# Performance work log

Hardware: AMD Instinct MI355X
Metric: run time of the kernel (lower is better)

## Reference

```python
import jax, jax.numpy as jnp
import numpy as np

N_NODES = 100000
N_EDGES = 1000000
IN_DIM = 64
OUT_DIM = 64


def setup_inputs() -> dict:
    key = jax.random.key(0)
    k1, k2, k3 = jax.random.split(key, 3)
    x = jax.random.normal(k1, (N_NODES, IN_DIM), dtype=jnp.float32)
    edge_index = jax.random.randint(k2, (2, N_EDGES), 0, N_NODES, dtype=jnp.int64)
    # PyG GCNConv linear weight [out_dim, in_dim] (glorot-ish scale) and bias
    W = jax.random.normal(k3, (OUT_DIM, IN_DIM), dtype=jnp.float32) * (1.0 / np.sqrt(IN_DIM))
    b = jnp.zeros((OUT_DIM,), dtype=jnp.float32)
    return {"x": x, "edge_index": edge_index, "W": W, "b": b}


def reference(x, edge_index, W, b):
    # GCNConv: add self-loops, symmetric deg^{-1/2} normalization,
    # linear transform, scatter-add aggregation, bias.
    # Dropout is identity in eval mode.
    N = x.shape[0]
    loop = jnp.arange(N, dtype=edge_index.dtype)
    src = jnp.concatenate([edge_index[0], loop])  # [E+N]
    dst = jnp.concatenate([edge_index[1], loop])  # [E+N]

    deg = jax.ops.segment_sum(jnp.ones_like(dst, dtype=x.dtype), dst, num_segments=N)
    dinv = jnp.where(deg > 0, jax.lax.rsqrt(deg), 0.0)  # [N]
    norm = dinv[src] * dinv[dst]                         # [E+N]

    h = x @ W.T                                          # [N, out_dim]
    msg = h[src] * norm[:, None]                         # gather + scale
    out = jax.ops.segment_sum(msg, dst, num_segments=N)  # scatter-add
    return out + b
```

## Files before the change

kernel.cpp:

```cpp
#include <hip/hip_runtime.h>

#define DIM 64
#define BIN_SHIFT 7
#define NODES_PER_BIN 128
#define MAX_BINS 1024
#define BIN_CAP 2048
#define CHUNK_EDGES 4096
#define SCATTER_THREADS 1024
#define GEMM_ROWS 128
#define FXSCALE 65536.0f
#define FXINV (1.0f / 65536.0f)
#define FXBIAS 524288u
#define MAGIC 12582912.0f
#define MAGIC_I 0x4B400000u
#define ACC_U64 33


using bf16x8 = __attribute__((ext_vector_type(8))) short;
using u16x8  = __attribute__((ext_vector_type(8))) unsigned short;
using f32x4  = __attribute__((ext_vector_type(4))) float;

__device__ __forceinline__ unsigned short f2bf(float f) {
    unsigned u = __float_as_uint(f);
    u += 0x7fffu + ((u >> 16) & 1u);
    return (unsigned short)(u >> 16);
}
__device__ __forceinline__ float bf2f(unsigned short u) {
    return __uint_as_float((unsigned)u << 16);
}
__device__ __forceinline__ unsigned fxq(unsigned short bf) {
    return __float_as_uint(fmaf(bf2f(bf), FXSCALE, MAGIC)) - (MAGIC_I - FXBIAS);
}

__global__ __launch_bounds__(SCATTER_THREADS) void bin_scatter_kernel(
    const void* __restrict__ ei, int* __restrict__ gcur,
    int* __restrict__ pairs, int E, int nbins) {
    __shared__ int h1[MAX_BINS];
    __shared__ int h2[MAX_BINS];
    __shared__ int base[MAX_BINS];
    __shared__ int s_notz;
    int tid = threadIdx.x;
    if (tid == 0) s_notz = 0;
    for (int i = tid; i < nbins; i += SCATTER_THREADS) { h1[i] = 0; h2[i] = 0; }
    __syncthreads();
    if (((const int*)ei)[2 * tid + 1] != 0) s_notz = 1;
    __syncthreads();
    int is64 = (s_notz == 0);
    int chunk = blockIdx.x * CHUNK_EDGES;

    int ss[CHUNK_EDGES / SCATTER_THREADS], dd[CHUNK_EDGES / SCATTER_THREADS];
#pragma unroll
    for (int k = 0; k < CHUNK_EDGES / SCATTER_THREADS; ++k) {
        int i = chunk + k * SCATTER_THREADS + tid;
        if (i < E) {
            int s, d;
            if (is64) {
                s = (int)((const long long*)ei)[i];
                d = (int)((const long long*)ei)[(long long)i + E];
            } else {
                s = ((const int*)ei)[i];
                d = ((const int*)ei)[i + E];
            }
            ss[k] = s; dd[k] = d;
            atomicAdd(&h1[d >> BIN_SHIFT], 1);
        } else {
            dd[k] = -1;
        }
    }
    __syncthreads();

    int myc = 0, ret = 0;
    if (tid < nbins) {
        myc = h1[tid];
        if (myc) ret = atomicAdd(&gcur[tid], myc);
    }
    int rk[CHUNK_EDGES / SCATTER_THREADS];
#pragma unroll
    for (int k = 0; k < CHUNK_EDGES / SCATTER_THREADS; ++k)
        if (dd[k] >= 0) rk[k] = atomicAdd(&h2[dd[k] >> BIN_SHIFT], 1);
    if (myc) base[tid] = tid * BIN_CAP + ret;
    __syncthreads();

#pragma unroll
    for (int k = 0; k < CHUNK_EDGES / SCATTER_THREADS; ++k) {
        if (dd[k] >= 0) {
            int bin = dd[k] >> BIN_SHIFT;
            int pos = base[bin] + rk[k];
            if (pos < (bin + 1) * BIN_CAP)
                pairs[pos] = (ss[k] << BIN_SHIFT) | (dd[k] & (NODES_PER_BIN - 1));
        }
    }
}

__global__ __launch_bounds__(256) void deg_gemm_kernel(
    const float* __restrict__ x, const float* __restrict__ W,
    const int* __restrict__ pairs, const int* __restrict__ gcur,
    int* __restrict__ deg, float* __restrict__ dinv,
    unsigned short* __restrict__ h, int N) {
    __shared__ unsigned short Xs[GEMM_ROWS * 64];
    __shared__ unsigned short Ws[64 * 64];
    __shared__ int sdeg[NODES_PER_BIN];
    __shared__ float sdinv[NODES_PER_BIN];
    int tid = threadIdx.x;
    int b = blockIdx.x;
    int row0 = b << BIN_SHIFT;
    int nn = min(GEMM_ROWS, N - row0);
    int cntb = min(gcur[b], BIN_CAP);

    if (tid < NODES_PER_BIN) sdeg[tid] = 0;
#pragma unroll
    for (int u = 0; u < 2; ++u) {
        int idx = u * 256 + tid;
        int c = idx >> 3, k0 = (idx & 7) * 8;
        float4 a = *(const float4*)&W[c * 64 + k0];
        float4 bb = *(const float4*)&W[c * 64 + k0 + 4];
        bf16x8 v;
        v[0] = (short)f2bf(a.x); v[1] = (short)f2bf(a.y);
        v[2] = (short)f2bf(a.z); v[3] = (short)f2bf(a.w);
        v[4] = (short)f2bf(bb.x); v[5] = (short)f2bf(bb.y);
        v[6] = (short)f2bf(bb.z); v[7] = (short)f2bf(bb.w);
        int byteoff = c * 128 + ((k0 * 2) ^ ((c & 7) << 4));
        *(bf16x8*)((char*)Ws + byteoff) = v;
    }
    const float* xbase = x + (size_t)row0 * DIM;
#pragma unroll
    for (int u = 0; u < 4; ++u) {
        int idx = u * 256 + tid;
        int r = idx >> 3, k0 = (idx & 7) * 8;
        float4 a = make_float4(0.f, 0.f, 0.f, 0.f), bb = a;
        if (r < nn) {
            a = *(const float4*)&xbase[r * DIM + k0];
            bb = *(const float4*)&xbase[r * DIM + k0 + 4];
        }
        bf16x8 v;
        v[0] = (short)f2bf(a.x); v[1] = (short)f2bf(a.y);
        v[2] = (short)f2bf(a.z); v[3] = (short)f2bf(a.w);
        v[4] = (short)f2bf(bb.x); v[5] = (short)f2bf(bb.y);
        v[6] = (short)f2bf(bb.z); v[7] = (short)f2bf(bb.w);
        int byteoff = r * 128 + ((k0 * 2) ^ ((r & 7) << 4));
        *(bf16x8*)((char*)Xs + byteoff) = v;
    }
    __syncthreads();
    const int* pb = pairs + b * BIN_CAP;
    for (int i = tid; i < cntb; i += 256)
        atomicAdd(&sdeg[pb[i] & (NODES_PER_BIN - 1)], 1);
    __syncthreads();
    if (tid < NODES_PER_BIN) {
        int d = sdeg[tid];
        float dv = rsqrtf((float)(d + 1));
        sdinv[tid] = dv;
        if (tid < nn) {
            deg[row0 + tid] = d;
            dinv[row0 + tid] = dv;
        }
    }
    __syncthreads();

    int w = tid >> 6, l = tid & 63;
    int lm = l & 15, kg = l >> 4;
    f32x4 acc[2][4] = {};
#pragma unroll
    for (int ks = 0; ks < 2; ++ks) {
        int kbyte = ks * 64 + kg * 16;
        int r0g = 32 * w + lm;
        int r1g = 32 * w + 16 + lm;
        bf16x8 a0 = *(const bf16x8*)((const char*)Xs + r0g * 128 + (kbyte ^ ((r0g & 7) << 4)));
        bf16x8 a1 = *(const bf16x8*)((const char*)Xs + r1g * 128 + (kbyte ^ ((r1g & 7) << 4)));
#pragma unroll
        for (int nt = 0; nt < 4; ++nt) {
            int ng = nt * 16 + lm;
            bf16x8 bv = *(const bf16x8*)((const char*)Ws + ng * 128 + (kbyte ^ ((ng & 7) << 4)));
            acc[0][nt] = __builtin_amdgcn_mfma_f32_16x16x32_bf16(a0, bv, acc[0][nt], 0, 0, 0);
            acc[1][nt] = __builtin_amdgcn_mfma_f32_16x16x32_bf16(a1, bv, acc[1][nt], 0, 0, 0);
        }
    }
#pragma unroll
    for (int mt = 0; mt < 2; ++mt) {
#pragma unroll
        for (int j = 0; j < 4; ++j) {
            int rl = 32 * w + 16 * mt + (l >> 4) * 4 + j;
            if (rl < nn) {
                float dv = sdinv[rl];
                size_t rowoff = (size_t)(row0 + rl) * DIM;
#pragma unroll
                for (int nt = 0; nt < 4; ++nt)
                    h[rowoff + nt * 16 + lm] = f2bf(acc[mt][nt][j] * dv);
            }
        }
    }
}

__global__ __launch_bounds__(512) void aggregate_kernel(
    const unsigned short* __restrict__ h, const int* __restrict__ pairs,
    const int* __restrict__ gcur, const int* __restrict__ deg,
    const float* __restrict__ dinv, const float* __restrict__ bias,
    float* __restrict__ out, int N) {
    __shared__ unsigned long long acc[NODES_PER_BIN * ACC_U64];
    int b = blockIdx.x;
    int tid = threadIdx.x;
    int cnt = min(gcur[b], BIN_CAP);
    int node0 = b << BIN_SHIFT;
    int nn = min(NODES_PER_BIN, N - node0);

    for (int i = tid; i < NODES_PER_BIN * ACC_U64; i += 512) acc[i] = 0ULL;
    __syncthreads();

    int wave = tid >> 6, lane = tid & 63;
    int g = lane >> 3;
    int fq = lane & 7;
    const int* pb = pairs + b * BIN_CAP;
    int dummy = N << BIN_SHIFT;

    for (int j0 = 64 * wave; j0 < cnt; j0 += 512) {
        int pk[8]; bool vd[8];
#pragma unroll
        for (int u = 0; u < 8; ++u) {
            int e = j0 + 8 * u + g;
            vd[u] = (e < cnt);
            pk[u] = vd[u] ? pb[e] : dummy;
        }
        u16x8 r[8];
#pragma unroll
        for (int u = 0; u < 8; ++u)
            r[u] = *(const u16x8*)(h + (size_t)(pk[u] >> BIN_SHIFT) * DIM + 8 * fq);
#pragma unroll
        for (int u = 0; u < 8; ++u) {
            unsigned q0 = fxq(r[u][0]), q1 = fxq(r[u][1]);
            unsigned q2 = fxq(r[u][2]), q3 = fxq(r[u][3]);
            unsigned q4 = fxq(r[u][4]), q5 = fxq(r[u][5]);
            unsigned q6 = fxq(r[u][6]), q7 = fxq(r[u][7]);
            if (vd[u]) {
                unsigned long long* ar =
                    &acc[(pk[u] & (NODES_PER_BIN - 1)) * ACC_U64 + 4 * fq];
                atomicAdd(&ar[0], (unsigned long long)q0 | ((unsigned long long)q1 << 32));
                atomicAdd(&ar[1], (unsigned long long)q2 | ((unsigned long long)q3 << 32));
                atomicAdd(&ar[2], (unsigned long long)q4 | ((unsigned long long)q5 << 32));
                atomicAdd(&ar[3], (unsigned long long)q6 | ((unsigned long long)q7 << 32));
            }
        }
    }
    __syncthreads();

    const int* accd = (const int*)acc;
    float bl = bias[lane];
    for (int n0 = wave; n0 < nn; n0 += 8) {
        int gn = node0 + n0;
        int dgn = deg[gn];
        float di = dinv[gn];
        unsigned q = (unsigned)accd[n0 * (2 * ACC_U64) + lane];
        int sfx = (int)(q - (unsigned)dgn * FXBIAS);
        float sum = (float)sfx * FXINV;
        float self = bf2f(h[(size_t)gn * DIM + lane]);
        out[(size_t)gn * DIM + lane] = (sum + self) * di + bl;
    }
}

extern "C" void kernel_launch(void* const* d_in, const int* in_sizes, int n_in,
                              void* d_out, int out_size, void* d_ws, size_t ws_size,
                              hipStream_t stream) {
    const float* x = (const float*)d_in[0];
    const void* ei = d_in[1];
    const float* W = (const float*)d_in[2];
    const float* b = (const float*)d_in[3];
    float* out = (float*)d_out;

    int N = in_sizes[0] / DIM;
    int E = in_sizes[1] / 2;
    int nbins = (N + NODES_PER_BIN - 1) >> BIN_SHIFT;

    char* ws = (char*)d_ws;
    auto align256 = [](size_t v) { return (v + 255) & ~(size_t)255; };
    size_t off = 0;
    int* gcur = (int*)(ws + off);              off = align256(off + (size_t)MAX_BINS * 4);
    int* deg  = (int*)(ws + off);              off = align256(off + (size_t)(N + 1) * 4);
    float* dinv = (float*)(ws + off);          off = align256(off + (size_t)(N + 1) * 4);
    int* pairs = (int*)(ws + off);             off = align256(off + ((size_t)nbins * BIN_CAP + 64) * 4);
    unsigned short* h = (unsigned short*)(ws + off); off = align256(off + (size_t)(N + 1) * DIM * 2);

    int nchunks = (E + CHUNK_EDGES - 1) / CHUNK_EDGES;

    hipMemsetAsync(gcur, 0, (size_t)MAX_BINS * 4, stream);
    bin_scatter_kernel<<<nchunks, SCATTER_THREADS, 0, stream>>>(ei, gcur, pairs, E, nbins);
    deg_gemm_kernel<<<nbins, 256, 0, stream>>>(x, W, pairs, gcur, deg, dinv, h, N);
    aggregate_kernel<<<nbins, 512, 0, stream>>>(h, pairs, gcur, deg, dinv, b, out, N);
}
```

Measured before the change: 126.6 us.

## Fuse scatter, GEMM and aggregation into one cooperative persistent kernel

Replaces the memset plus three-kernel pipeline with a single cooperative kernel that uses grid-wide syncs between the binning, degree/GEMM and aggregation phases. One block per bin also does its share of edge binning and computes the GEMM before the first grid sync, so that work overlaps with the scatter. Degree and dinv stay in shared memory rather than global arrays. The cost is three grid barriers, occupancy limited so every bin fits co-resident, and a fallback to the old path if cooperative launch is unavailable.

```diff
diff --git a/kernel.cpp b/kernel.cpp
--- a/kernel.cpp
+++ b/kernel.cpp
@@ -1,4 +1,7 @@
 #include <hip/hip_runtime.h>
+#include <hip/hip_cooperative_groups.h>
+
+namespace cg = cooperative_groups;
 
 #define DIM 64
 #define BIN_SHIFT 7
@@ -7,13 +10,13 @@
 #define BIN_CAP 2048
 #define CHUNK_EDGES 4096
 #define SCATTER_THREADS 1024
-#define GEMM_ROWS 128
 #define FXSCALE 65536.0f
 #define FXINV (1.0f / 65536.0f)
 #define FXBIAS 524288u
 #define MAGIC 12582912.0f
 #define MAGIC_I 0x4B400000u
 #define ACC_U64 33
+#define FSLOTS 5
 
 
 using bf16x8 = __attribute__((ext_vector_type(8))) short;
@@ -30,6 +33,220 @@
 }
 __device__ __forceinline__ unsigned fxq(unsigned short bf) {
     return __float_as_uint(fmaf(bf2f(bf), FXSCALE, MAGIC)) - (MAGIC_I - FXBIAS);
+}
+
+union SmemU {
+    struct { unsigned short Xs[NODES_PER_BIN * 64]; unsigned short Ws[64 * 64]; } g;
+    int base[MAX_BINS];
+    unsigned long long acc[NODES_PER_BIN * ACC_U64];
+};
+
+__global__ __launch_bounds__(256, 4) void fused_kernel(
+    const void* __restrict__ ei, const float* __restrict__ x,
+    const float* __restrict__ W, const float* __restrict__ bias,
+    int* __restrict__ gcur, int* __restrict__ pairs,
+    unsigned short* __restrict__ h, float* __restrict__ out,
+    int E, int N, int nbins, int chunk) {
+    cg::grid_group grid = cg::this_grid();
+    __shared__ int h1[MAX_BINS];
+    __shared__ SmemU u;
+    __shared__ int sdeg[NODES_PER_BIN];
+    __shared__ float sdinv[NODES_PER_BIN];
+    __shared__ int s_notz;
+
+    int tid = threadIdx.x;
+    int b = blockIdx.x;
+    int node0 = b << BIN_SHIFT;
+    int nn = min(NODES_PER_BIN, N - node0);
+    int w = tid >> 6, l = tid & 63;
+    int lm = l & 15, kg = l >> 4;
+
+    if (tid == 0) { s_notz = 0; gcur[b] = 0; }
+    for (int i = tid; i < nbins; i += 256) h1[i] = 0;
+    __syncthreads();
+    if (((const int*)ei)[2 * tid + 1] != 0) s_notz = 1;
+    __syncthreads();
+    int is64 = (s_notz == 0);
+
+    int e0 = b * chunk;
+    int e1 = min(e0 + chunk, E);
+    int ss[FSLOTS], dd[FSLOTS];
+#pragma unroll
+    for (int k = 0; k < FSLOTS; ++k) {
+        int i = e0 + k * 256 + tid;
+        dd[k] = -1;
+        if (i < e1) {
+            if (is64) {
+                ss[k] = (int)((const long long*)ei)[i];
+                dd[k] = (int)((const long long*)ei)[(long long)i + E];
+            } else {
+                ss[k] = ((const int*)ei)[i];
+                dd[k] = ((const int*)ei)[i + E];
+            }
+            atomicAdd(&h1[dd[k] >> BIN_SHIFT], 1);
+        }
+    }
+#pragma unroll
+    for (int uu = 0; uu < 2; ++uu) {
+        int idx = uu * 256 + tid;
+        int c = idx >> 3, k0 = (idx & 7) * 8;
+        float4 a = *(const float4*)&W[c * 64 + k0];
+        float4 bb = *(const float4*)&W[c * 64 + k0 + 4];
+        bf16x8 v;
+        v[0] = (short)f2bf(a.x); v[1] = (short)f2bf(a.y);
+        v[2] = (short)f2bf(a.z); v[3] = (short)f2bf(a.w);
+        v[4] = (short)f2bf(bb.x); v[5] = (short)f2bf(bb.y);
+        v[6] = (short)f2bf(bb.z); v[7] = (short)f2bf(bb.w);
+        int byteoff = c * 128 + ((k0 * 2) ^ ((c & 7) << 4));
+        *(bf16x8*)((char*)u.g.Ws + byteoff) = v;
+    }
+    const float* xbase = x + (size_t)node0 * DIM;
+#pragma unroll
+    for (int uu = 0; uu < 4; ++uu) {
+        int idx = uu * 256 + tid;
+        int r = idx >> 3, k0 = (idx & 7) * 8;
+        float4 a = make_float4(0.f, 0.f, 0.f, 0.f), bb = a;
+        if (r < nn) {
+            a = *(const float4*)&xbase[r * DIM + k0];
+            bb = *(const float4*)&xbase[r * DIM + k0 + 4];
+        }
+        bf16x8 v;
+        v[0] = (short)f2bf(a.x); v[1] = (short)f2bf(a.y);
+        v[2] = (short)f2bf(a.z); v[3] = (short)f2bf(a.w);
+        v[4] = (short)f2bf(bb.x); v[5] = (short)f2bf(bb.y);
+        v[6] = (short)f2bf(bb.z); v[7] = (short)f2bf(bb.w);
+        int byteoff = r * 128 + ((k0 * 2) ^ ((r & 7) << 4));
+        *(bf16x8*)((char*)u.g.Xs + byteoff) = v;
+    }
+    __syncthreads();
+
+    f32x4 racc[2][4] = {};
+#pragma unroll
+    for (int ks = 0; ks < 2; ++ks) {
+        int kbyte = ks * 64 + kg * 16;
+        int r0g = 32 * w + lm;
+        int r1g = 32 * w + 16 + lm;
+        bf16x8 a0 = *(const bf16x8*)((const char*)u.g.Xs + r0g * 128 + (kbyte ^ ((r0g & 7) << 4)));
+        bf16x8 a1 = *(const bf16x8*)((const char*)u.g.Xs + r1g * 128 + (kbyte ^ ((r1g & 7) << 4)));
+#pragma unroll
+        for (int nt = 0; nt < 4; ++nt) {
+            int ng = nt * 16 + lm;
+            bf16x8 bv = *(const bf16x8*)((const char*)u.g.Ws + ng * 128 + (kbyte ^ ((ng & 7) << 4)));
+            racc[0][nt] = __builtin_amdgcn_mfma_f32_16x16x32_bf16(a0, bv, racc[0][nt], 0, 0, 0);
+            racc[1][nt] = __builtin_amdgcn_mfma_f32_16x16x32_bf16(a1, bv, racc[1][nt], 0, 0, 0);
+        }
+    }
+    grid.sync();
+
+    int myc[4] = {0, 0, 0, 0}, ret[4] = {0, 0, 0, 0};
+#pragma unroll
+    for (int j = 0; j < 4; ++j) {
+        int i = tid + j * 256;
+        if (i < nbins) myc[j] = h1[i];
+    }
+    __syncthreads();
+    for (int i = tid; i < nbins; i += 256) h1[i] = 0;
+    __syncthreads();
+#pragma unroll
+    for (int j = 0; j < 4; ++j) {
+        int i = tid + j * 256;
+        if (i < nbins && myc[j]) ret[j] = atomicAdd(&gcur[i], myc[j]);
+    }
+    int rk[FSLOTS];
+#pragma unroll
+    for (int k = 0; k < FSLOTS; ++k)
+        if (dd[k] >= 0) rk[k] = atomicAdd(&h1[dd[k] >> BIN_SHIFT], 1);
+#pragma unroll
+    for (int j = 0; j < 4; ++j) {
+        int i = tid + j * 256;
+        if (i < nbins && myc[j]) u.base[i] = i * BIN_CAP + ret[j];
+    }
+    __syncthreads();
+#pragma unroll
+    for (int k = 0; k < FSLOTS; ++k) {
+        if (dd[k] >= 0) {
+            int bin = dd[k] >> BIN_SHIFT;
+            int pos = u.base[bin] + rk[k];
+            if (pos < (bin + 1) * BIN_CAP)
+                pairs[pos] = (ss[k] << BIN_SHIFT) | (dd[k] & (NODES_PER_BIN - 1));
+        }
+    }
+    grid.sync();
+
+    int cnt = min(gcur[b], BIN_CAP);
+    if (tid < NODES_PER_BIN) sdeg[tid] = 0;
+    __syncthreads();
+    const int* pb = pairs + b * BIN_CAP;
+    for (int i = tid; i < cnt; i += 256)
+        atomicAdd(&sdeg[pb[i] & (NODES_PER_BIN - 1)], 1);
+    __syncthreads();
+    if (tid < NODES_PER_BIN)
+        sdinv[tid] = rsqrtf((float)(sdeg[tid] + 1));
+    __syncthreads();
+#pragma unroll
+    for (int mt = 0; mt < 2; ++mt) {
+#pragma unroll
+        for (int j = 0; j < 4; ++j) {
+            int rl = 32 * w + 16 * mt + (l >> 4) * 4 + j;
+            if (rl < nn) {
+                float dv = sdinv[rl];
+                size_t rowoff = (size_t)(node0 + rl) * DIM;
+#pragma unroll
+                for (int nt = 0; nt < 4; ++nt)
+                    h[rowoff + nt * 16 + lm] = f2bf(racc[mt][nt][j] * dv);
+            }
+        }
+    }
+    grid.sync();
+
+    for (int i = tid; i < NODES_PER_BIN * ACC_U64; i += 256) u.acc[i] = 0ULL;
+    __syncthreads();
+    int g = l >> 3;
+    int fq = l & 7;
+    int dummy = N << BIN_SHIFT;
+
+    for (int j0 = 64 * w; j0 < cnt; j0 += 256) {
+        int pk[8]; bool vd[8];
+#pragma unroll
+        for (int uu = 0; uu < 8; ++uu) {
+            int e = j0 + 8 * uu + g;
+            vd[uu] = (e < cnt);
+            pk[uu] = vd[uu] ? pb[e] : dummy;
+        }
+        u16x8 r[8];
+#pragma unroll
+        for (int uu = 0; uu < 8; ++uu)
+            r[uu] = *(const u16x8*)(h + (size_t)(pk[uu] >> BIN_SHIFT) * DIM + 8 * fq);
+#pragma unroll
+        for (int uu = 0; uu < 8; ++uu) {
+            unsigned q0 = fxq(r[uu][0]), q1 = fxq(r[uu][1]);
+            unsigned q2 = fxq(r[uu][2]), q3 = fxq(r[uu][3]);
+            unsigned q4 = fxq(r[uu][4]), q5 = fxq(r[uu][5]);
+            unsigned q6 = fxq(r[uu][6]), q7 = fxq(r[uu][7]);
+            if (vd[uu]) {
+                unsigned long long* ar =
+                    &u.acc[(pk[uu] & (NODES_PER_BIN - 1)) * ACC_U64 + 4 * fq];
+                atomicAdd(&ar[0], (unsigned long long)q0 | ((unsigned long long)q1 << 32));
+                atomicAdd(&ar[1], (unsigned long long)q2 | ((unsigned long long)q3 << 32));
+                atomicAdd(&ar[2], (unsigned long long)q4 | ((unsigned long long)q5 << 32));
+                atomicAdd(&ar[3], (unsigned long long)q6 | ((unsigned long long)q7 << 32));
+            }
+        }
+    }
+    __syncthreads();
+
+    const int* accd = (const int*)u.acc;
+    float bl = bias[l];
+    for (int n0 = w; n0 < nn; n0 += 4) {
+        int gn = node0 + n0;
+        int dgn = sdeg[n0];
+        float di = sdinv[n0];
+        unsigned q = (unsigned)accd[n0 * (2 * ACC_U64) + l];
+        int sfx = (int)(q - (unsigned)dgn * FXBIAS);
+        float sum = (float)sfx * FXINV;
+        float self = bf2f(h[(size_t)gn * DIM + l]);
+        out[(size_t)gn * DIM + l] = (sum + self) * di + bl;
+    }
 }
 
 __global__ __launch_bounds__(SCATTER_THREADS) void bin_scatter_kernel(
@@ -47,42 +264,36 @@
     __syncthreads();
     int is64 = (s_notz == 0);
     int chunk = blockIdx.x * CHUNK_EDGES;
-
-    int ss[CHUNK_EDGES / SCATTER_THREADS], dd[CHUNK_EDGES / SCATTER_THREADS];
-#pragma unroll
-    for (int k = 0; k < CHUNK_EDGES / SCATTER_THREADS; ++k) {
+    int ss[4], dd[4];
+#pragma unroll
+    for (int k = 0; k < 4; ++k) {
         int i = chunk + k * SCATTER_THREADS + tid;
+        dd[k] = -1;
         if (i < E) {
-            int s, d;
             if (is64) {
-                s = (int)((const long long*)ei)[i];
-                d = (int)((const long long*)ei)[(long long)i + E];
+                ss[k] = (int)((const long long*)ei)[i];
+                dd[k] = (int)((const long long*)ei)[(long long)i + E];
             } else {
-                s = ((const int*)ei)[i];
-                d = ((const int*)ei)[i + E];
+                ss[k] = ((const int*)ei)[i];
+                dd[k] = ((const int*)ei)[i + E];
             }
-            ss[k] = s; dd[k] = d;
-            atomicAdd(&h1[d >> BIN_SHIFT], 1);
-        } else {
-            dd[k] = -1;
-        }
-    }
-    __syncthreads();
-
+            atomicAdd(&h1[dd[k] >> BIN_SHIFT], 1);
+        }
+    }
+    __syncthreads();
     int myc = 0, ret = 0;
     if (tid < nbins) {
         myc = h1[tid];
         if (myc) ret = atomicAdd(&gcur[tid], myc);
     }
-    int rk[CHUNK_EDGES / SCATTER_THREADS];
-#pragma unroll
-    for (int k = 0; k < CHUNK_EDGES / SCATTER_THREADS; ++k)
+    int rk[4];
+#pragma unroll
+    for (int k = 0; k < 4; ++k)
         if (dd[k] >= 0) rk[k] = atomicAdd(&h2[dd[k] >> BIN_SHIFT], 1);
     if (myc) base[tid] = tid * BIN_CAP + ret;
     __syncthreads();
-
-#pragma unroll
-    for (int k = 0; k < CHUNK_EDGES / SCATTER_THREADS; ++k) {
+#pragma unroll
+    for (int k = 0; k < 4; ++k) {
         if (dd[k] >= 0) {
             int bin = dd[k] >> BIN_SHIFT;
             int pos = base[bin] + rk[k];
@@ -97,14 +308,14 @@
     const int* __restrict__ pairs, const int* __restrict__ gcur,
     int* __restrict__ deg, float* __restrict__ dinv,
     unsigned short* __restrict__ h, int N) {
-    __shared__ unsigned short Xs[GEMM_ROWS * 64];
+    __shared__ unsigned short Xs[NODES_PER_BIN * 64];
     __shared__ unsigned short Ws[64 * 64];
     __shared__ int sdeg[NODES_PER_BIN];
     __shared__ float sdinv[NODES_PER_BIN];
     int tid = threadIdx.x;
     int b = blockIdx.x;
     int row0 = b << BIN_SHIFT;
-    int nn = min(GEMM_ROWS, N - row0);
+    int nn = min(NODES_PER_BIN, N - row0);
     int cntb = min(gcur[b], BIN_CAP);
 
     if (tid < NODES_PER_BIN) sdeg[tid] = 0;
@@ -261,12 +472,13 @@
     const float* x = (const float*)d_in[0];
     const void* ei = d_in[1];
     const float* W = (const float*)d_in[2];
-    const float* b = (const float*)d_in[3];
+    const float* bias = (const float*)d_in[3];
     float* out = (float*)d_out;
 
     int N = in_sizes[0] / DIM;
     int E = in_sizes[1] / 2;
     int nbins = (N + NODES_PER_BIN - 1) >> BIN_SHIFT;
+    int chunk = ((E + nbins - 1) / nbins + 255) & ~255;
 
     char* ws = (char*)d_ws;
     auto align256 = [](size_t v) { return (v + 255) & ~(size_t)255; };
@@ -277,10 +489,31 @@
     int* pairs = (int*)(ws + off);             off = align256(off + ((size_t)nbins * BIN_CAP + 64) * 4);
     unsigned short* h = (unsigned short*)(ws + off); off = align256(off + (size_t)(N + 1) * DIM * 2);
 
+    static int s_use_coop = -1;
+    if (s_use_coop < 0) {
+        int dev = 0, coop = 0, ncu = 0, maxb = 0;
+        (void)hipGetDevice(&dev);
+        (void)hipDeviceGetAttribute(&coop, hipDeviceAttributeCooperativeLaunch, dev);
+        (void)hipDeviceGetAttribute(&ncu, hipDeviceAttributeMultiprocessorCount, dev);
+        (void)hipOccupancyMaxActiveBlocksPerMultiprocessor(&maxb, (const void*)fused_kernel, 256, 0);
+        s_use_coop = (coop && (long long)maxb * ncu >= nbins) ? 1 : 0;
+    }
+
+    if (s_use_coop) {
+        void* args[] = {
+            (void*)&ei, (void*)&x, (void*)&W, (void*)&bias,
+            (void*)&gcur, (void*)&pairs, (void*)&h, (void*)&out,
+            (void*)&E, (void*)&N, (void*)&nbins, (void*)&chunk
+        };
+        hipError_t err = hipLaunchCooperativeKernel((const void*)fused_kernel,
+                                                    dim3(nbins), dim3(256), args, 0, stream);
+        if (err == hipSuccess) return;
+        s_use_coop = 0;
+    }
+
     int nchunks = (E + CHUNK_EDGES - 1) / CHUNK_EDGES;
-
     hipMemsetAsync(gcur, 0, (size_t)MAX_BINS * 4, stream);
     bin_scatter_kernel<<<nchunks, SCATTER_THREADS, 0, stream>>>(ei, gcur, pairs, E, nbins);
     deg_gemm_kernel<<<nbins, 256, 0, stream>>>(x, W, pairs, gcur, deg, dinv, h, N);
-    aggregate_kernel<<<nbins, 512, 0, stream>>>(h, pairs, gcur, deg, dinv, b, out, N);
-}
+    aggregate_kernel<<<nbins, 512, 0, stream>>>(h, pairs, gcur, deg, dinv, bias, out, N);
+}
```

Result: faster. 124.1 us (-2.0%).
